# Kernel optimization log

Measured on AMD Instinct MI355X. Metric: run time of the kernel, lower is better.

## Reference

```python
import jax, jax.numpy as jnp
import numpy as np

B, V, N, IN_F, HEADS, OUT_F = 4, 4, 1000, 64, 4, 32
D = HEADS * OUT_F  # 128, concat=True
E = 64000
NEG_SLOPE = 0.2


def setup_inputs() -> dict:
    key = jax.random.key(0)
    ks = jax.random.split(key, 8)
    x = jax.random.normal(ks[0], (B, V, N, IN_F), jnp.float32)
    edge_index = jax.random.randint(ks[1], (2, E), 0, B * N, dtype=jnp.int64)
    W = jax.random.normal(ks[2], (HEADS * OUT_F, IN_F), jnp.float32) / np.sqrt(IN_F)
    att = jax.random.normal(ks[3], (1, HEADS, 2 * OUT_F), jnp.float32) * 0.1
    in_proj_w = jax.random.normal(ks[4], (3 * D, D), jnp.float32) / np.sqrt(D)
    in_proj_b = jnp.zeros((3 * D,), jnp.float32)
    out_proj_w = jax.random.normal(ks[5], (D, D), jnp.float32) / np.sqrt(D)
    out_proj_b = jnp.zeros((D,), jnp.float32)
    bias = jnp.zeros((D,), jnp.float32)
    return dict(x=x, W=W, att=att, in_proj_w=in_proj_w, in_proj_b=in_proj_b,
                out_proj_w=out_proj_w, out_proj_b=out_proj_b, bias=bias,
                edge_index=edge_index)


def reference(x, W, att, in_proj_w, in_proj_b, out_proj_w, out_proj_b, bias, edge_index):
    Bx, Vx, Nx, _ = x.shape
    Ntot = Bx * Nx
    # intra-view GAT: shared W across views
    h = jnp.einsum('bvni,oi->bvno', x, W).reshape(Bx, Vx, Nx, HEADS, OUT_F)
    # block-diagonal placement: h_full[b*V+v, b*N:(b+1)*N] = h[b,v]
    ib = jnp.arange(Bx)
    hf = jnp.zeros((Bx, Vx, Bx, Nx, HEADS, OUT_F), x.dtype).at[ib, :, ib].set(h)
    h_full = hf.reshape(Bx * Vx, Ntot, HEADS, OUT_F)
    # add self loops
    loops = jnp.arange(Ntot, dtype=edge_index.dtype)
    src = jnp.concatenate([edge_index[0], loops])
    dst = jnp.concatenate([edge_index[1], loops])
    # attention scores (faithful to source: flatten h_full over (B*V, Ntot) and
    # index with raw node ids, i.e. gathers from block 0 only)
    h_flat = h_full.reshape(Bx * Vx * Ntot, HEADS, OUT_F)
    h_cat = jnp.concatenate([h_flat[src], h_flat[dst]], axis=-1)  # [Etot, H, 2*OUT]
    att_in = jax.nn.leaky_relu(h_cat, NEG_SLOPE)
    scores = jnp.sum(att * att_in, axis=-1)  # [Etot, HEADS]
    # per-destination segment softmax
    seg_max = jax.ops.segment_max(scores, dst, num_segments=Ntot)
    seg_max = jax.lax.stop_gradient(jnp.where(jnp.isfinite(seg_max), seg_max, 0.0))
    ex = jnp.exp(scores - seg_max[dst])
    denom = jax.ops.segment_sum(ex, dst, num_segments=Ntot)
    alpha = ex / (denom[dst] + 1e-16)  # [Etot, HEADS]
    # scatter-add aggregation, broadcast over B*V rows
    msgs = h_full[:, src] * alpha[None, :, :, None]  # [B*V, Etot, H, OUT]
    out_full = jnp.zeros_like(h_full).at[:, dst].add(msgs)
    # extract each graph's own node block
    out = out_full.reshape(Bx, Vx, Bx, Nx, HEADS, OUT_F)[ib, :, ib]  # [B,V,N,H,OUT]
    h_gat = out.reshape(Bx, Vx, Nx, HEADS * OUT_F)  # concat heads
    # inter-view mixing: MHA over the V axis per node
    seq = h_gat.transpose(0, 2, 1, 3).reshape(Bx * Nx, Vx, D)
    q, k, v = jnp.split(seq @ in_proj_w.T + in_proj_b, 3, axis=-1)
    hd = D // HEADS
    sp = lambda t: t.reshape(Bx * Nx, Vx, HEADS, hd).transpose(0, 2, 1, 3)
    q, k, v = sp(q), sp(k), sp(v)
    aw = jax.nn.softmax(jnp.einsum('bhqd,bhkd->bhqk', q, k) / jnp.sqrt(jnp.asarray(hd, x.dtype)), axis=-1)
    ao = jnp.einsum('bhqk,bhkd->bhqd', aw, v).transpose(0, 2, 1, 3).reshape(Bx * Nx, Vx, D)
    mixed = ao @ out_proj_w.T + out_proj_b
    h_mixed = mixed.reshape(Bx, Nx, Vx, D).transpose(0, 2, 1, 3)  # [B,V,N,D]
    return h_mixed + bias
```

## Files before the change

kernel.cpp:

```cpp
#include <hip/hip_runtime.h>

#define NN 1000
#define HEADS_ 4
#define DM 128
#define EE 64000
#define NTOT 4000
#define ETOT 68000
#define CAP 48
#define EB 34

__device__ void gemm64_k1(float* As, float* Bs, int mi, int ni,
                          const float* __restrict__ x, const float* __restrict__ W,
                          float* __restrict__ hbuf, const float* __restrict__ att,
                          float* __restrict__ ssrc, float* __restrict__ sdst) {
  int tid = threadIdx.x;
  int m0 = mi * 64, n0 = ni * 64;
  int tx = tid & 15, ty = tid >> 4;
  const float4* A4 = (const float4*)x;
  const float4* W4 = (const float4*)W;
  float acc[4][4] = {};

  __syncthreads();
  {
    int q = tid & 15, r0 = tid >> 4;
#pragma unroll
    for (int p = 0; p < 4; ++p) {
      int r = r0 + p * 16;
      float4 v = A4[(size_t)(m0 + r) * 16 + q];
      *(float4*)&As[r * 64 + ((q ^ ((r >> 2) & 15)) << 2)] = v;
    }
#pragma unroll
    for (int p = 0; p < 4; ++p) {
      int r = r0 + p * 16;
      float4 v = W4[(size_t)(n0 + r) * 16 + q];
      *(float4*)&Bs[r * 64 + ((q ^ ((r >> 2) & 15)) << 2)] = v;
    }
  }
  __syncthreads();
#pragma unroll 4
  for (int q = 0; q < 16; ++q) {
    float4 a[4], b[4];
    int sa = (q ^ ty) << 2;
    int sb = (q ^ tx) << 2;
#pragma unroll
    for (int i = 0; i < 4; ++i)
      a[i] = *(const float4*)&As[(ty * 4 + i) * 64 + sa];
#pragma unroll
    for (int j = 0; j < 4; ++j)
      b[j] = *(const float4*)&Bs[(tx * 4 + j) * 64 + sb];
#pragma unroll
    for (int i = 0; i < 4; ++i)
#pragma unroll
      for (int j = 0; j < 4; ++j)
        acc[i][j] += a[i].x * b[j].x + a[i].y * b[j].y
                   + a[i].z * b[j].z + a[i].w * b[j].w;
  }

  int nc = n0 + tx * 4;
#pragma unroll
  for (int i = 0; i < 4; ++i) {
    int m = m0 + ty * 4 + i;
    *(float4*)&hbuf[(size_t)m * DM + nc] =
        make_float4(acc[i][0], acc[i][1], acc[i][2], acc[i][3]);
  }

  if (m0 < NN) {
    int hsel = tx >> 3;
    int h = ni * 2 + hsel;
    int kb = (tx & 7) * 4;
    float a0[4], a1[4];
#pragma unroll
    for (int j = 0; j < 4; ++j) {
      a0[j] = att[h * 64 + kb + j];
      a1[j] = att[h * 64 + 32 + kb + j];
    }
#pragma unroll
    for (int i = 0; i < 4; ++i) {
      int m = m0 + ty * 4 + i;
      float p0 = 0.f, p1 = 0.f;
#pragma unroll
      for (int j = 0; j < 4; ++j) {
        float g = acc[i][j];
        float lr = g > 0.f ? g : 0.2f * g;
        p0 += a0[j] * lr;
        p1 += a1[j] * lr;
      }
      p0 += __shfl_xor(p0, 1, 16); p1 += __shfl_xor(p1, 1, 16);
      p0 += __shfl_xor(p0, 2, 16); p1 += __shfl_xor(p1, 2, 16);
      p0 += __shfl_xor(p0, 4, 16); p1 += __shfl_xor(p1, 4, 16);
      if ((tx & 7) == 0 && m < NN) {
        ssrc[m * HEADS_ + h] = p0;
        sdst[m * HEADS_ + h] = p1;
      }
    }
  }
}

__global__ __launch_bounds__(256) void k1_kernel(const float* __restrict__ x,
                                                 const float* __restrict__ W,
                                                 const float* __restrict__ att,
                                                 float* __restrict__ hbuf,
                                                 float* __restrict__ ssrc,
                                                 float* __restrict__ sdst,
                                                 const int* __restrict__ ei,
                                                 int* __restrict__ cnt,
                                                 int* __restrict__ elist) {
  __shared__ float smem[8192];
  int bid = blockIdx.x;
  if (bid < 500) {
    gemm64_k1(smem, smem + 4096, bid >> 1, bid & 1, x, W, hbuf, att, ssrc, sdst);
  } else {
    for (int e = (bid - 500) * 256 + threadIdx.x; e < ETOT; e += EB * 256) {
      int s, d;
      if (e < EE) { s = ei[e]; d = ei[EE + e]; }
      else { s = d = e - EE; }
      int pos = atomicAdd(&cnt[d], 1);
      if (pos < CAP) elist[d * CAP + pos] = s;
    }
  }
}

__global__ __launch_bounds__(512) void mega3_kernel(const int* __restrict__ cnt,
                                                    const int* __restrict__ elist,
                                                    const float* __restrict__ ssrc,
                                                    const float* __restrict__ sdst,
                                                    const float* __restrict__ hbuf,
                                                    const float* __restrict__ inw,
                                                    const float* __restrict__ inb,
                                                    const float* __restrict__ outw,
                                                    const float* __restrict__ outb,
                                                    const float* __restrict__ bias,
                                                    float* __restrict__ out) {
  __shared__ float smem[12416];
  float* As    = smem;
  float* rg2   = smem + 4224;
  float* exsF  = rg2;
  int*   srcsI = (int*)(rg2 + 1536);
  float* Bs    = rg2;
  float* Bs2   = rg2;
  float* aoS   = smem;

  int tid = threadIdx.x;
  int g0n = blockIdx.x * 8;

  {
    int ln = tid >> 6, t64 = tid & 63;
    int d = g0n + ln;
    int m = cnt[d]; if (m > CAP) m = CAP;
    float sd = (d < NN) ? sdst[d * HEADS_ + (t64 & 3)] : 0.f;
    for (int base = 0; base < m; base += 16) {
      int i = base + (t64 >> 2);
      if (i < m) {
        int s = elist[d * CAP + i];
        if ((t64 & 3) == 0) srcsI[ln * CAP + i] = s;
        float ss = (s < NN) ? ssrc[s * HEADS_ + (t64 & 3)] : 0.f;
        exsF[ln * 192 + i * 4 + (t64 & 3)] = __expf(ss + sd);
      }
    }
  }
  __syncthreads();

  {
    int r = tid >> 4, f = tid & 15;
    int ln = r >> 2, v = r & 3;
    int d = g0n + ln, b = d / NN;
    int m = cnt[d]; if (m > CAP) m = CAP;
    int h_lo = f >> 3, h_hi = 2 + (f >> 3);
    const float* hbase = hbuf + ((size_t)(b * 4 + v) * NN) * DM + f * 4;
    float4 alo = make_float4(0.f, 0.f, 0.f, 0.f), ahi = alo;
    float dlo = 1e-16f, dhi = 1e-16f;
    int i = 0;
    for (; i + 4 <= m; i += 4) {
      float exl[4], exh[4]; unsigned sl[4]; const float* hrow[4];
#pragma unroll
      for (int u = 0; u < 4; ++u) {
        exl[u] = exsF[ln * 192 + (i + u) * 4 + h_lo];
        exh[u] = exsF[ln * 192 + (i + u) * 4 + h_hi];
        sl[u] = (unsigned)(srcsI[ln * CAP + i + u] - b * NN);
        unsigned sc = sl[u] < NN ? sl[u] : 0u;
        hrow[u] = hbase + (size_t)sc * DM;
      }
      float4 hl[4], hh[4];
#pragma unroll
      for (int u = 0; u < 4; ++u) {
        hl[u] = *(const float4*)(hrow[u]);
        hh[u] = *(const float4*)(hrow[u] + 64);
      }
#pragma unroll
      for (int u = 0; u < 4; ++u) {
        dlo += exl[u]; dhi += exh[u];
        float wl = sl[u] < NN ? exl[u] : 0.f, wh = sl[u] < NN ? exh[u] : 0.f;
        alo.x += wl * hl[u].x; alo.y += wl * hl[u].y;
        alo.z += wl * hl[u].z; alo.w += wl * hl[u].w;
        ahi.x += wh * hh[u].x; ahi.y += wh * hh[u].y;
        ahi.z += wh * hh[u].z; ahi.w += wh * hh[u].w;
      }
    }
    for (; i < m; ++i) {
      float exl = exsF[ln * 192 + i * 4 + h_lo];
      float exh = exsF[ln * 192 + i * 4 + h_hi];
      unsigned sl = (unsigned)(srcsI[ln * CAP + i] - b * NN);
      unsigned sc = sl < NN ? sl : 0u;
      const float* hrow = hbase + (size_t)sc * DM;
      float4 hl = *(const float4*)(hrow);
      float4 hh = *(const float4*)(hrow + 64);
      dlo += exl; dhi += exh;
      float wl = sl < NN ? exl : 0.f, wh = sl < NN ? exh : 0.f;
      alo.x += wl * hl.x; alo.y += wl * hl.y; alo.z += wl * hl.z; alo.w += wl * hl.w;
      ahi.x += wh * hh.x; ahi.y += wh * hh.y; ahi.z += wh * hh.z; ahi.w += wh * hh.w;
    }
    float il = 1.f / dlo, ih = 1.f / dhi;
    *(float4*)&As[r * 132 +      f * 4] = make_float4(alo.x * il, alo.y * il, alo.z * il, alo.w * il);
    *(float4*)&As[r * 132 + 64 + f * 4] = make_float4(ahi.x * ih, ahi.y * ih, ahi.z * ih, ahi.w * ih);
  }
  __syncthreads();

  int tx = tid & 63, ty = tid >> 6;
  float acc[3][4][2] = {};
  {
    const float4* W4 = (const float4*)inw;
#pragma unroll
    for (int c = 0; c < 2; ++c) {
#pragma unroll
      for (int ni = 0; ni < 3; ++ni) {
        __syncthreads();
        {
          int q = tid & 15, r0 = tid >> 4;
#pragma unroll
          for (int p = 0; p < 4; ++p) {
            int r = r0 + p * 32;
            float4 v = W4[(size_t)(ni * 128 + r) * 32 + c * 16 + q];
            *(float4*)&Bs[r * 64 + ((q ^ ((r >> 2) & 15)) << 2)] = v;
          }
        }
        __syncthreads();
#pragma unroll 4
        for (int q = 0; q < 16; ++q) {
          float4 a[4], b[2];
#pragma unroll
          for (int i = 0; i < 4; ++i)
            a[i] = *(const float4*)&As[(ty * 4 + i) * 132 + c * 64 + q * 4];
#pragma unroll
          for (int j = 0; j < 2; ++j) {
            int rn = tx * 2 + j;
            b[j] = *(const float4*)&Bs[rn * 64 + ((q ^ ((rn >> 2) & 15)) << 2)];
          }
#pragma unroll
          for (int i = 0; i < 4; ++i)
#pragma unroll
            for (int j = 0; j < 2; ++j)
              acc[ni][i][j] += a[i].x * b[j].x + a[i].y * b[j].y
                             + a[i].z * b[j].z + a[i].w * b[j].w;
        }
      }
    }
  }

#pragma unroll
  for (int ni = 0; ni < 3; ++ni) {
    float b0 = inb[ni * 128 + tx * 2], b1 = inb[ni * 128 + tx * 2 + 1];
#pragma unroll
    for (int i = 0; i < 4; ++i) { acc[ni][i][0] += b0; acc[ni][i][1] += b1; }
  }
  float S[4][4];
#pragma unroll
  for (int vq = 0; vq < 4; ++vq)
#pragma unroll
    for (int vk = 0; vk < 4; ++vk)
      S[vq][vk] = acc[0][vq][0] * acc[1][vk][0] + acc[0][vq][1] * acc[1][vk][1];
#pragma unroll
  for (int vq = 0; vq < 4; ++vq)
#pragma unroll
    for (int vk = 0; vk < 4; ++vk) {
      float s = S[vq][vk];
      s += __shfl_xor(s, 1);
      s += __shfl_xor(s, 2);
      s += __shfl_xor(s, 4);
      s += __shfl_xor(s, 8);
      S[vq][vk] = s * 0.17677669529663687f;
    }
#pragma unroll
  for (int vq = 0; vq < 4; ++vq) {
    float mx = fmaxf(fmaxf(S[vq][0], S[vq][1]), fmaxf(S[vq][2], S[vq][3]));
    float e0 = __expf(S[vq][0] - mx), e1 = __expf(S[vq][1] - mx);
    float e2 = __expf(S[vq][2] - mx), e3 = __expf(S[vq][3] - mx);
    float inv = 1.f / (e0 + e1 + e2 + e3);
    S[vq][0] = e0 * inv; S[vq][1] = e1 * inv; S[vq][2] = e2 * inv; S[vq][3] = e3 * inv;
  }
  float ao0[4], ao1[4];
#pragma unroll
  for (int vq = 0; vq < 4; ++vq) {
    ao0[vq] = S[vq][0] * acc[2][0][0] + S[vq][1] * acc[2][1][0]
            + S[vq][2] * acc[2][2][0] + S[vq][3] * acc[2][3][0];
    ao1[vq] = S[vq][0] * acc[2][0][1] + S[vq][1] * acc[2][1][1]
            + S[vq][2] * acc[2][2][1] + S[vq][3] * acc[2][3][1];
  }
  __syncthreads();
  {
#pragma unroll
    for (int vq = 0; vq < 4; ++vq) {
      float2 w2 = make_float2(ao0[vq], ao1[vq]);
      *(float2*)&aoS[(ty * 4 + vq) * 132 + tx * 2] = w2;
    }
  }

  float oc[4][2] = {};
  const float4* O4 = (const float4*)outw;
#pragma unroll
  for (int c = 0; c < 2; ++c) {
    {
      int q = tid & 15, r0 = tid >> 4;
#pragma unroll
      for (int p = 0; p < 4; ++p) {
        int r = r0 + p * 32;
        float4 v = O4[(size_t)r * 32 + c * 16 + q];
        *(float4*)&Bs2[r * 64 + ((q ^ ((r >> 2) & 15)) << 2)] = v;
      }
    }
    __syncthreads();
#pragma unroll 4
    for (int q = 0; q < 16; ++q) {
      float4 a[4], bq[2];
#pragma unroll
      for (int i = 0; i < 4; ++i)
        a[i] = *(const float4*)&aoS[(ty * 4 + i) * 132 + c * 64 + q * 4];
#pragma unroll
      for (int j = 0; j < 2; ++j) {
        int rn = tx * 2 + j;
        bq[j] = *(const float4*)&Bs2[rn * 64 + ((q ^ ((rn >> 2) & 15)) << 2)];
      }
#pragma unroll
      for (int i = 0; i < 4; ++i)
#pragma unroll
        for (int j = 0; j < 2; ++j)
          oc[i][j] += a[i].x * bq[j].x + a[i].y * bq[j].y
                    + a[i].z * bq[j].z + a[i].w * bq[j].w;
    }
    __syncthreads();
  }

  {
    int nc = tx * 2;
    float o0 = outb[nc] + bias[nc], o1 = outb[nc + 1] + bias[nc + 1];
#pragma unroll
    for (int i = 0; i < 4; ++i) {
      int node = g0n + ty, vv = i;
      int bg = node / NN, n = node - bg * NN;
      int om = (bg * 4 + vv) * NN + n;
      *(float2*)&out[(size_t)om * DM + nc] = make_float2(oc[i][0] + o0, oc[i][1] + o1);
    }
  }
}

extern "C" void kernel_launch(void* const* d_in, const int* in_sizes, int n_in,
                              void* d_out, int out_size, void* d_ws, size_t ws_size,
                              hipStream_t stream) {
  const float* x    = (const float*)d_in[0];
  const float* W    = (const float*)d_in[1];
  const float* att  = (const float*)d_in[2];
  const float* inw  = (const float*)d_in[3];
  const float* inb  = (const float*)d_in[4];
  const float* outw = (const float*)d_in[5];
  const float* outb = (const float*)d_in[6];
  const float* bias = (const float*)d_in[7];
  const int*   ei   = (const int*)d_in[8];
  float* out = (float*)d_out;

  float* ws = (float*)d_ws;
  float* hbuf  = ws;
  float* ssrc  = ws + 12500000;
  float* sdst  = ssrc + 16000;
  int*   cnt   = (int*)(sdst + 16000);
  int*   elist = cnt + 4000;

  hipMemsetAsync(cnt, 0, 4000 * sizeof(int), stream);

  k1_kernel<<<500 + EB, 256, 0, stream>>>(x, W, att, hbuf, ssrc, sdst, ei, cnt, elist);
  mega3_kernel<<<NTOT / 8, 512, 0, stream>>>(cnt, elist, ssrc, sdst, hbuf,
                                             inw, inb, outw, outb, bias, out);
}
```

Before: 141.4 us.

## Pre-transpose projection weights and read them directly from global in fused mixing kernel

The first kernel gains extra blocks that transpose the MHA in-projection and out-projection weights into workspace. The fused aggregation and mixing kernel drops the shared-memory staging of weight tiles, along with their barriers, and streams the transposed weights straight from global or L2 with coalesced float2 reads. Blocks shrink from 8 nodes and 512 threads to 4 nodes and 256 threads with far less LDS, which should allow more resident blocks per CU. The cost is redundant weight traffic from every block through cache, and the per-call transpose is extra work inside the timed launch.

```diff
diff --git a/kernel.cpp b/kernel.cpp
--- a/kernel.cpp
+++ b/kernel.cpp
@@ -8,6 +8,7 @@
 #define ETOT 68000
 #define CAP 48
 #define EB 34
+#define TB 10
 
 __device__ void gemm64_k1(float* As, float* Bs, int mi, int ni,
                           const float* __restrict__ x, const float* __restrict__ W,
@@ -104,12 +105,16 @@
                                                  float* __restrict__ sdst,
                                                  const int* __restrict__ ei,
                                                  int* __restrict__ cnt,
-                                                 int* __restrict__ elist) {
+                                                 int* __restrict__ elist,
+                                                 const float* __restrict__ inw,
+                                                 const float* __restrict__ outw,
+                                                 float* __restrict__ inwT,
+                                                 float* __restrict__ outwT) {
   __shared__ float smem[8192];
   int bid = blockIdx.x;
   if (bid < 500) {
     gemm64_k1(smem, smem + 4096, bid >> 1, bid & 1, x, W, hbuf, att, ssrc, sdst);
-  } else {
+  } else if (bid < 500 + EB) {
     for (int e = (bid - 500) * 256 + threadIdx.x; e < ETOT; e += EB * 256) {
       int s, d;
       if (e < EE) { s = ei[e]; d = ei[EE + e]; }
@@ -117,31 +122,43 @@
       int pos = atomicAdd(&cnt[d], 1);
       if (pos < CAP) elist[d * CAP + pos] = s;
     }
+  } else {
+    int tb = bid - (500 + EB);
+    if (tb < 8) {
+      for (int g = tb * 6144 + threadIdx.x; g < (tb + 1) * 6144; g += 256) {
+        int col = g >> 7, k = g & 127;
+        inwT[k * 384 + col] = inw[(size_t)col * 128 + k];
+      }
+    } else {
+      int ob = tb - 8;
+      for (int g = ob * 8192 + threadIdx.x; g < (ob + 1) * 8192; g += 256) {
+        int col = g >> 7, k = g & 127;
+        outwT[k * 128 + col] = outw[(size_t)col * 128 + k];
+      }
+    }
   }
 }
 
-__global__ __launch_bounds__(512) void mega3_kernel(const int* __restrict__ cnt,
+__global__ __launch_bounds__(256) void mega2_kernel(const int* __restrict__ cnt,
                                                     const int* __restrict__ elist,
                                                     const float* __restrict__ ssrc,
                                                     const float* __restrict__ sdst,
                                                     const float* __restrict__ hbuf,
-                                                    const float* __restrict__ inw,
+                                                    const float* __restrict__ inwT,
                                                     const float* __restrict__ inb,
-                                                    const float* __restrict__ outw,
+                                                    const float* __restrict__ outwT,
                                                     const float* __restrict__ outb,
                                                     const float* __restrict__ bias,
                                                     float* __restrict__ out) {
-  __shared__ float smem[12416];
+  __shared__ float smem[3136];
   float* As    = smem;
-  float* rg2   = smem + 4224;
-  float* exsF  = rg2;
-  int*   srcsI = (int*)(rg2 + 1536);
-  float* Bs    = rg2;
-  float* Bs2   = rg2;
+  float* exsF  = smem + 2112;
+  int*   srcsI = (int*)(smem + 2112 + 768);
   float* aoS   = smem;
 
   int tid = threadIdx.x;
-  int g0n = blockIdx.x * 8;
+  int g0n = blockIdx.x * 4;
+  int kgN = (int)(blockDim.x >> 3);
 
   {
     int ln = tid >> 6, t64 = tid & 63;
@@ -218,39 +235,32 @@
   int tx = tid & 63, ty = tid >> 6;
   float acc[3][4][2] = {};
   {
-    const float4* W4 = (const float4*)inw;
-#pragma unroll
-    for (int c = 0; c < 2; ++c) {
-#pragma unroll
-      for (int ni = 0; ni < 3; ++ni) {
-        __syncthreads();
-        {
-          int q = tid & 15, r0 = tid >> 4;
-#pragma unroll
-          for (int p = 0; p < 4; ++p) {
-            int r = r0 + p * 32;
-            float4 v = W4[(size_t)(ni * 128 + r) * 32 + c * 16 + q];
-            *(float4*)&Bs[r * 64 + ((q ^ ((r >> 2) & 15)) << 2)] = v;
+    const float2* BT = (const float2*)inwT;
+    for (int kg = 0; kg < kgN; ++kg) {
+      float4 a4[4];
+#pragma unroll
+      for (int i = 0; i < 4; ++i)
+        a4[i] = *(const float4*)&As[(ty * 4 + i) * 132 + kg * 4];
+      float2 bb[12];
+#pragma unroll
+      for (int kk = 0; kk < 4; ++kk)
+#pragma unroll
+        for (int p = 0; p < 3; ++p)
+          bb[kk * 3 + p] = BT[(size_t)(kg * 4 + kk) * 192 + p * 64 + tx];
+#pragma unroll
+      for (int kk = 0; kk < 4; ++kk) {
+        float av[4];
+#pragma unroll
+        for (int i = 0; i < 4; ++i)
+          av[i] = kk == 0 ? a4[i].x : kk == 1 ? a4[i].y : kk == 2 ? a4[i].z : a4[i].w;
+#pragma unroll
+        for (int p = 0; p < 3; ++p) {
+          float2 b = bb[kk * 3 + p];
+#pragma unroll
+          for (int i = 0; i < 4; ++i) {
+            acc[p][i][0] += av[i] * b.x;
+            acc[p][i][1] += av[i] * b.y;
           }
-        }
-        __syncthreads();
-#pragma unroll 4
-        for (int q = 0; q < 16; ++q) {
-          float4 a[4], b[2];
-#pragma unroll
-          for (int i = 0; i < 4; ++i)
-            a[i] = *(const float4*)&As[(ty * 4 + i) * 132 + c * 64 + q * 4];
-#pragma unroll
-          for (int j = 0; j < 2; ++j) {
-            int rn = tx * 2 + j;
-            b[j] = *(const float4*)&Bs[rn * 64 + ((q ^ ((rn >> 2) & 15)) << 2)];
-          }
-#pragma unroll
-          for (int i = 0; i < 4; ++i)
-#pragma unroll
-            for (int j = 0; j < 2; ++j)
-              acc[ni][i][j] += a[i].x * b[j].x + a[i].y * b[j].y
-                             + a[i].z * b[j].z + a[i].w * b[j].w;
         }
       }
     }
@@ -296,47 +306,37 @@
             + S[vq][2] * acc[2][2][1] + S[vq][3] * acc[2][3][1];
   }
   __syncthreads();
-  {
-#pragma unroll
-    for (int vq = 0; vq < 4; ++vq) {
-      float2 w2 = make_float2(ao0[vq], ao1[vq]);
-      *(float2*)&aoS[(ty * 4 + vq) * 132 + tx * 2] = w2;
-    }
-  }
+#pragma unroll
+  for (int vq = 0; vq < 4; ++vq)
+    *(float2*)&aoS[(ty * 4 + vq) * 132 + tx * 2] = make_float2(ao0[vq], ao1[vq]);
+  __syncthreads();
 
   float oc[4][2] = {};
-  const float4* O4 = (const float4*)outw;
-#pragma unroll
-  for (int c = 0; c < 2; ++c) {
-    {
-      int q = tid & 15, r0 = tid >> 4;
-#pragma unroll
-      for (int p = 0; p < 4; ++p) {
-        int r = r0 + p * 32;
-        float4 v = O4[(size_t)r * 32 + c * 16 + q];
-        *(float4*)&Bs2[r * 64 + ((q ^ ((r >> 2) & 15)) << 2)] = v;
-      }
-    }
-    __syncthreads();
-#pragma unroll 4
-    for (int q = 0; q < 16; ++q) {
-      float4 a[4], bq[2];
+  {
+    const float2* OT = (const float2*)outwT;
+    for (int kg = 0; kg < kgN; ++kg) {
+      float4 a4[4];
 #pragma unroll
       for (int i = 0; i < 4; ++i)
-        a[i] = *(const float4*)&aoS[(ty * 4 + i) * 132 + c * 64 + q * 4];
-#pragma unroll
-      for (int j = 0; j < 2; ++j) {
-        int rn = tx * 2 + j;
-        bq[j] = *(const float4*)&Bs2[rn * 64 + ((q ^ ((rn >> 2) & 15)) << 2)];
-      }
-#pragma unroll
-      for (int i = 0; i < 4; ++i)
-#pragma unroll
-        for (int j = 0; j < 2; ++j)
-          oc[i][j] += a[i].x * bq[j].x + a[i].y * bq[j].y
-                    + a[i].z * bq[j].z + a[i].w * bq[j].w;
-    }
-    __syncthreads();
+        a4[i] = *(const float4*)&aoS[(ty * 4 + i) * 132 + kg * 4];
+      float2 bb[4];
+#pragma unroll
+      for (int kk = 0; kk < 4; ++kk)
+        bb[kk] = OT[(size_t)(kg * 4 + kk) * 64 + tx];
+#pragma unroll
+      for (int kk = 0; kk < 4; ++kk) {
+        float av[4];
+#pragma unroll
+        for (int i = 0; i < 4; ++i)
+          av[i] = kk == 0 ? a4[i].x : kk == 1 ? a4[i].y : kk == 2 ? a4[i].z : a4[i].w;
+        float2 b = bb[kk];
+#pragma unroll
+        for (int i = 0; i < 4; ++i) {
+          oc[i][0] += av[i] * b.x;
+          oc[i][1] += av[i] * b.y;
+        }
+      }
+    }
   }
 
   {
@@ -372,10 +372,14 @@
   float* sdst  = ssrc + 16000;
   int*   cnt   = (int*)(sdst + 16000);
   int*   elist = cnt + 4000;
+  float* inwT  = ws + 12800000;
+  float* outwT = ws + 12900000;
 
   hipMemsetAsync(cnt, 0, 4000 * sizeof(int), stream);
 
-  k1_kernel<<<500 + EB, 256, 0, stream>>>(x, W, att, hbuf, ssrc, sdst, ei, cnt, elist);
-  mega3_kernel<<<NTOT / 8, 512, 0, stream>>>(cnt, elist, ssrc, sdst, hbuf,
-                                             inw, inb, outw, outb, bias, out);
+  k1_kernel<<<500 + EB + TB, 256, 0, stream>>>(x, W, att, hbuf, ssrc, sdst,
+                                               ei, cnt, elist, inw, outw,
+                                               inwT, outwT);
+  mega2_kernel<<<NTOT / 4, 256, 0, stream>>>(cnt, elist, ssrc, sdst, hbuf,
+                                             inwT, inb, outwT, outb, bias, out);
 }
```

Measured after the change: 157.9 us. +11.6%, slower.
